# Performance work log

Hardware: AMD Instinct MI355X
Metric: run time of the kernel (lower is better)

## Reference

```python
import jax, jax.numpy as jnp
import numpy as np

B, T, J, C, H = 128, 512, 21, 3, 64


def setup_inputs() -> dict:
    key = jax.random.key(0)
    ks = jax.random.split(key, 14)
    x = jax.random.normal(ks[0], (B, T, J, C), dtype=jnp.float32)
    # Fixed skeleton-like adjacency buffer: symmetric, self-loops, row-normalized.
    A = (jax.random.uniform(ks[1], (J, J)) < 0.15).astype(jnp.float32)
    A = jnp.clip(A + A.T, 0.0, 1.0) + jnp.eye(J, dtype=jnp.float32)
    A = A / A.sum(axis=1, keepdims=True)
    s = 0.05
    W1 = jax.random.normal(ks[2], (H, C), jnp.float32) * s
    b1 = jnp.zeros((H,), jnp.float32)
    W2 = jax.random.normal(ks[3], (H, H), jnp.float32) * s
    b2 = jnp.zeros((H,), jnp.float32)
    Wa = jax.random.normal(ks[4], (1, H), jnp.float32) * s
    ba = jnp.zeros((1,), jnp.float32)
    W_ih = jax.random.normal(ks[5], (3 * H, J * H), jnp.float32) * s
    b_ih = jnp.zeros((3 * H,), jnp.float32)
    W_hh = jax.random.normal(ks[6], (3 * H, H), jnp.float32) * s
    b_hh = jnp.zeros((3 * H,), jnp.float32)
    W_head = jax.random.normal(ks[7], (J * C, H), jnp.float32) * s
    b_head = jnp.zeros((J * C,), jnp.float32)
    return {"x": x, "A": A, "W1": W1, "b1": b1, "W2": W2, "b2": b2,
            "Wa": Wa, "ba": ba, "W_ih": W_ih, "b_ih": b_ih,
            "W_hh": W_hh, "b_hh": b_hh, "W_head": W_head, "b_head": b_head}


def _gcn(A, x, W, b):
    # aggregated = einsum('ij,btjc->btic'); then Linear + ReLU
    agg = jnp.einsum('ij,btjc->btic', A, x)
    return jax.nn.relu(agg @ W.T + b)


def reference(x, A, W1, b1, W2, b2, Wa, ba, W_ih, b_ih, W_hh, b_hh, W_head, b_head):
    h = _gcn(A, x, W1, b1)            # (B,T,J,H)
    h = _gcn(A, h, W2, b2)            # (B,T,J,H)
    # Spatial attention: per-node score, mean over time, softmax over joints
    scores = (h @ Wa.T + ba).mean(axis=1)        # (B,J,1)
    attn = jax.nn.softmax(scores, axis=1)        # (B,J,1)
    h = h * attn[:, None]                        # (B,T,J,H)
    b_, t_, j_, c_ = h.shape
    seq = h.reshape(b_, t_, j_ * c_)             # (B,T,J*H)
    # GRU (PyTorch convention). Precompute input projections outside the scan.
    xproj = seq @ W_ih.T + b_ih                  # (B,T,3H)
    h0 = jnp.zeros((b_, H), xproj.dtype)

    def step(hprev, xp):
        gh = hprev @ W_hh.T + b_hh
        xr, xz, xn = jnp.split(xp, 3, axis=-1)
        hr, hz, hn = jnp.split(gh, 3, axis=-1)
        r = jax.nn.sigmoid(xr + hr)
        z = jax.nn.sigmoid(xz + hz)
        n = jnp.tanh(xn + r * hn)
        hnew = (1.0 - z) * n + z * hprev
        return hnew, None

    hT, _ = jax.lax.scan(step, h0, jnp.swapaxes(xproj, 0, 1))  # last hidden state
    out = hT @ W_head.T + b_head                 # (B, J*C)
    return out, attn.squeeze(-1)
```

## Files before the change

kernel.cpp:

```cpp
#include <hip/hip_runtime.h>
#include <cstdint>
#include <cstddef>

#define NB 128
#define NT 512
#define NJ 21
#define NC 3
#define NH 64
#define JH 1344
#define G3 192
#define OUT0 (NB*NJ*NC)
#define FB 4

typedef __attribute__((ext_vector_type(8))) __bf16 bf16x8;
typedef __attribute__((ext_vector_type(4))) float f32x4;

__device__ __forceinline__ float bf2f(unsigned short u) {
  union { unsigned int i; float f; } v; v.i = ((unsigned int)u) << 16; return v.f;
}
__device__ __forceinline__ unsigned short f2bf(float f) {
  union { float f; unsigned int i; } v; v.f = f;
  unsigned int x = v.i;
  unsigned int lsb = (x >> 16) & 1u;
  x += 0x7fffu + lsb;
  return (unsigned short)(x >> 16);
}
__device__ __forceinline__ unsigned int pk_bf16(float lo, float hi) {
  unsigned int r;
  asm("v_cvt_pk_bf16_f32 %0, %1, %2" : "=v"(r) : "v"(lo), "v"(hi));
  return r;
}
__device__ __forceinline__ unsigned int scale2(unsigned int u, float s) {
  float lo = __uint_as_float(u << 16);
  float hi = __uint_as_float(u & 0xffff0000u);
  return pk_bf16(lo * s, hi * s);
}

__global__ __launch_bounds__(256) void k0_convw(
    const float* __restrict__ W, unsigned short* __restrict__ Wbf) {
  const int ti = blockIdx.x*256 + threadIdx.x;
  const float4 v = ((const float4*)W)[ti];
  uint2 o;
  o.x = (unsigned int)f2bf(v.x) | ((unsigned int)f2bf(v.y) << 16);
  o.y = (unsigned int)f2bf(v.z) | ((unsigned int)f2bf(v.w) << 16);
  ((uint2*)Wbf)[ti] = o;
}

__global__ __launch_bounds__(256, 2) void k1_fused(
    const float* __restrict__ x, const float* __restrict__ A,
    const float* __restrict__ W1, const float* __restrict__ b1,
    const float* __restrict__ W2, const float* __restrict__ b2,
    const float* __restrict__ Wa,
    unsigned short* __restrict__ h2out, float* __restrict__ scorepart) {
  __shared__ unsigned short h1s[FB*32*72];
  __shared__ unsigned short us[FB*64*40];
  __shared__ unsigned short w2s[64*72];
  __shared__ unsigned short adjs[32*40];
  __shared__ unsigned short h2st[FB*NJ*72];
  __shared__ float afs[NJ*NJ];
  __shared__ float xs[4][64];
  __shared__ float ags[4][64];
  __shared__ float spred[4][NJ];

  const int tid = threadIdx.x;
  const int w = tid >> 6, l = tid & 63;
  const int q = l >> 4, r = l & 15;
  const int b = blockIdx.x >> 7, ch = blockIdx.x & 127;
  const int t0 = ch * FB;

  for (int i = tid; i < NJ*NJ; i += 256) afs[i] = A[i];
  for (int i = tid; i < 1024; i += 256) {
    const int ii = i >> 5, jj = i & 31;
    adjs[ii*40 + jj] = (ii < NJ && jj < NJ) ? f2bf(A[ii*NJ + jj]) : (unsigned short)0;
  }
  {
    const int h = tid & 63, qd = tid >> 6;
    const int g0 = qd * 16;
#pragma unroll
    for (int e = 0; e < 16; e += 2) {
      const float v0 = W2[h*64 + g0 + e], v1 = W2[h*64 + g0 + e + 1];
      ((unsigned int*)w2s)[h*36 + ((g0 + e) >> 1)] = pk_bf16(v0, v1);
    }
  }
#pragma unroll
  for (int j = NJ; j < 32; ++j)
    ((unsigned int*)h1s)[(w*32 + j)*36 + (l & 31)] = 0u;

  const float w1r0 = W1[l*3+0], w1r1 = W1[l*3+1], w1r2 = W1[l*3+2];
  const float b1h = b1[l];
  float b2v[4][4], wav[4][4];
#pragma unroll
  for (int mt = 0; mt < 4; ++mt)
#pragma unroll
    for (int rg = 0; rg < 4; ++rg) {
      const int h = mt*16 + q*4 + rg;
      b2v[mt][rg] = b2[h]; wav[mt][rg] = Wa[h];
    }
  __syncthreads();

  {
    const size_t fr = (size_t)(b*NT + t0 + w);
    if (l < NJ*NC) xs[w][l] = x[fr*(NJ*NC) + l];
    if (l < NJ*NC) {
      const int ji = l / 3, c = l - ji*3;
      float s = 0.f;
#pragma unroll
      for (int j = 0; j < NJ; ++j) s += afs[ji*NJ + j] * xs[w][j*3 + c];
      ags[w][l] = s;
    }
#pragma unroll
    for (int j = 0; j < NJ; ++j) {
      float v = b1h + w1r0*ags[w][j*3+0] + w1r1*ags[w][j*3+1] + w1r2*ags[w][j*3+2];
      v = fmaxf(v, 0.f);
      h1s[(w*32 + j)*72 + l] = f2bf(v);
    }
  }
  __syncthreads();

  bf16x8 bw[2][4];
#pragma unroll
  for (int ks = 0; ks < 2; ++ks)
#pragma unroll
    for (int nt = 0; nt < 4; ++nt)
      bw[ks][nt] = *(const bf16x8*)(&w2s[(nt*16 + r)*72 + (ks*4 + q)*8]);
  f32x4 acc1[2][4];
#pragma unroll
  for (int i = 0; i < 2; ++i)
#pragma unroll
    for (int j2 = 0; j2 < 4; ++j2) acc1[i][j2] = (f32x4)0.f;
#pragma unroll
  for (int mti = 0; mti < 2; ++mti) {
    const int row = (w*2 + mti)*16 + r;
#pragma unroll
    for (int ks = 0; ks < 2; ++ks) {
      const bf16x8 af = *(const bf16x8*)(&h1s[row*72 + (ks*4 + q)*8]);
#pragma unroll
      for (int nt = 0; nt < 4; ++nt)
        acc1[mti][nt] = __builtin_amdgcn_mfma_f32_16x16x32_bf16(af, bw[ks][nt], acc1[mti][nt], 0,0,0);
    }
  }
#pragma unroll
  for (int mti = 0; mti < 2; ++mti)
#pragma unroll
    for (int nt = 0; nt < 4; ++nt) {
      const int h = nt*16 + r;
#pragma unroll
      for (int rp = 0; rp < 2; ++rp) {
        const int jp = mti*16 + q*4 + rp*2;
        ((unsigned int*)us)[(w*64 + h)*20 + (jp >> 1)] =
            pk_bf16(acc1[mti][nt][rp*2], acc1[mti][nt][rp*2+1]);
      }
    }
  __syncthreads();

  bf16x8 badj[2];
#pragma unroll
  for (int nt = 0; nt < 2; ++nt)
    badj[nt] = *(const bf16x8*)(&adjs[(nt*16 + r)*40 + q*8]);
  f32x4 acc2[4][2];
#pragma unroll
  for (int i = 0; i < 4; ++i) { acc2[i][0] = (f32x4)0.f; acc2[i][1] = (f32x4)0.f; }
#pragma unroll
  for (int mt = 0; mt < 4; ++mt) {
    const int h = mt*16 + r;
    const bf16x8 af = *(const bf16x8*)(&us[(w*64 + h)*40 + q*8]);
#pragma unroll
    for (int nt = 0; nt < 2; ++nt)
      acc2[mt][nt] = __builtin_amdgcn_mfma_f32_16x16x32_bf16(af, badj[nt], acc2[mt][nt], 0,0,0);
  }
  float sp0 = 0.f, sp1 = 0.f;
#pragma unroll
  for (int nt = 0; nt < 2; ++nt) {
    const int i = nt*16 + r;
    if (i < NJ) {
#pragma unroll
      for (int mt = 0; mt < 4; ++mt)
#pragma unroll
        for (int rp = 0; rp < 2; ++rp) {
          const int h0 = mt*16 + q*4 + rp*2;
          const float v0 = fmaxf(acc2[mt][nt][rp*2]   + b2v[mt][rp*2],   0.f);
          const float v1 = fmaxf(acc2[mt][nt][rp*2+1] + b2v[mt][rp*2+1], 0.f);
          if (nt == 0) sp0 += v0*wav[mt][rp*2] + v1*wav[mt][rp*2+1];
          else         sp1 += v0*wav[mt][rp*2] + v1*wav[mt][rp*2+1];
          ((unsigned int*)h2st)[(w*NJ + i)*36 + (h0 >> 1)] = pk_bf16(v0, v1);
        }
    }
  }
  sp0 += __shfl_xor(sp0, 16); sp0 += __shfl_xor(sp0, 32);
  sp1 += __shfl_xor(sp1, 16); sp1 += __shfl_xor(sp1, 32);
  if (l < 16) spred[w][l] = sp0;
  if (l < 5)  spred[w][16 + l] = sp1;
  __syncthreads();

  if (tid < NJ)
    scorepart[((size_t)b*128 + ch)*NJ + tid] =
      spred[0][tid] + spred[1][tid] + spred[2][tid] + spred[3][tid];

  const size_t gbase = (size_t)(b*NT + t0) * JH;
  for (int cid = tid; cid < FB*NJ*8; cid += 256) {
    const int f = cid / (NJ*8), rem = cid - f*(NJ*8);
    const int i = rem >> 3, p = rem & 7;
    const uint4 v = *(const uint4*)(&h2st[(f*NJ + i)*72 + p*8]);
    *(uint4*)(&h2out[gbase + (size_t)f*JH + i*64 + p*8]) = v;
  }
}

__global__ __launch_bounds__(64) void k2_attn(
    const float* __restrict__ scorepart, float* __restrict__ attn,
    float* __restrict__ out_attn) {
  __shared__ float ss[NJ];
  const int b = blockIdx.x, tid = threadIdx.x;
  if (tid < NJ) {
    float s = 0.f;
    for (int ch = 0; ch < 128; ++ch) s += scorepart[(b*128 + ch)*NJ + tid];
    ss[tid] = s * (1.0f/NT);
  }
  __syncthreads();
  float m = -1e30f;
  for (int j = 0; j < NJ; ++j) m = fmaxf(m, ss[j]);
  float sum = 0.f;
  for (int j = 0; j < NJ; ++j) sum += expf(ss[j] - m);
  if (tid < NJ) {
    float a = expf(ss[tid] - m) / sum;
    attn[b*NJ + tid] = a;
    out_attn[b*NJ + tid] = a;
  }
}

__global__ __launch_bounds__(256, 2) void k3_xproj_mfma(
    const unsigned short* __restrict__ h2, const unsigned short* __restrict__ Wbf,
    const float* __restrict__ b_ih, const float* __restrict__ b_hh,
    const float* __restrict__ attn, float* __restrict__ xproj) {
  __shared__ unsigned short Abuf[2][128*32];
  __shared__ unsigned short Bbuf[2][192*32];
  const int tid = threadIdx.x;
  const int w = tid >> 6, l = tid & 63;
  const int lq = l >> 4, lr = l & 15;
  const int blk = blockIdx.x;
  const int b = blk >> 2;
  const int t0 = (blk & 3) << 7;
  const int wm = w >> 1, wn = w & 1;

  const unsigned short* gA[2]; int ldsA[2];
#pragma unroll
  for (int i = 0; i < 2; ++i) {
    const int lc = tid*2 + i, rr = lc >> 2, j = lc & 3;
    gA[i] = h2 + (size_t)(b*NT + t0 + rr)*JH + j*8;
    ldsA[i] = rr*32 + ((j ^ ((rr>>1)&3)) << 3);
  }
  const unsigned short* gB[3]; int ldsB[3];
#pragma unroll
  for (int i = 0; i < 3; ++i) {
    const int lc = tid + 256*i, g = lc >> 2, j = lc & 3;
    gB[i] = Wbf + (size_t)g*JH + j*8;
    ldsB[i] = g*32 + ((j ^ ((g>>1)&3)) << 3);
  }
  int aoff[4], boff[6];
#pragma unroll
  for (int mt = 0; mt < 4; ++mt) {
    const int row = wm*64 + mt*16 + lr;
    aoff[mt] = row*32 + ((lq ^ ((row>>1)&3)) << 3);
  }
#pragma unroll
  for (int nt = 0; nt < 6; ++nt) {
    const int g = wn*96 + nt*16 + lr;
    boff[nt] = g*32 + ((lq ^ ((g>>1)&3)) << 3);
  }

  f32x4 acc[4][6];
#pragma unroll
  for (int mt = 0; mt < 4; ++mt)
#pragma unroll
    for (int nt = 0; nt < 6; ++nt) acc[mt][nt] = (f32x4)0.f;

  {
    const float s = attn[b*NJ + 0];
#pragma unroll
    for (int i = 0; i < 2; ++i)
      *(uint4*)(&Abuf[0][ldsA[i]]) = *(const uint4*)(gA[i]);
#pragma unroll
    for (int i = 0; i < 3; ++i) {
      uint4 v = *(const uint4*)(gB[i]);
      v.x = scale2(v.x, s); v.y = scale2(v.y, s);
      v.z = scale2(v.z, s); v.w = scale2(v.w, s);
      *(uint4*)(&Bbuf[0][ldsB[i]]) = v;
    }
  }
  __syncthreads();

  for (int ks = 0; ks < 42; ++ks) {
    const int cur = ks & 1;
    uint4 av0, av1, bv0, bv1, bv2;
    if (ks < 41) {
      const int kk = (ks+1)*32;
      av0 = *(const uint4*)(gA[0] + kk);
      av1 = *(const uint4*)(gA[1] + kk);
      bv0 = *(const uint4*)(gB[0] + kk);
      bv1 = *(const uint4*)(gB[1] + kk);
      bv2 = *(const uint4*)(gB[2] + kk);
    }
    bf16x8 af[4], bfr[6];
#pragma unroll
    for (int mt = 0; mt < 4; ++mt) af[mt] = *(const bf16x8*)(&Abuf[cur][aoff[mt]]);
#pragma unroll
    for (int nt = 0; nt < 6; ++nt) bfr[nt] = *(const bf16x8*)(&Bbuf[cur][boff[nt]]);
#pragma unroll
    for (int mt = 0; mt < 4; ++mt)
#pragma unroll
      for (int nt = 0; nt < 6; ++nt)
        acc[mt][nt] = __builtin_amdgcn_mfma_f32_16x16x32_bf16(af[mt], bfr[nt], acc[mt][nt], 0, 0, 0);
    if (ks < 41) {
      const float s = attn[b*NJ + ((ks+1) >> 1)];
      *(uint4*)(&Abuf[cur^1][ldsA[0]]) = av0;
      *(uint4*)(&Abuf[cur^1][ldsA[1]]) = av1;
      uint4 v;
      v = bv0; v.x = scale2(v.x, s); v.y = scale2(v.y, s); v.z = scale2(v.z, s); v.w = scale2(v.w, s);
      *(uint4*)(&Bbuf[cur^1][ldsB[0]]) = v;
      v = bv1; v.x = scale2(v.x, s); v.y = scale2(v.y, s); v.z = scale2(v.z, s); v.w = scale2(v.w, s);
      *(uint4*)(&Bbuf[cur^1][ldsB[1]]) = v;
      v = bv2; v.x = scale2(v.x, s); v.y = scale2(v.y, s); v.z = scale2(v.z, s); v.w = scale2(v.w, s);
      *(uint4*)(&Bbuf[cur^1][ldsB[2]]) = v;
    }
    __syncthreads();
  }

  float bias[6];
#pragma unroll
  for (int nt = 0; nt < 6; ++nt) {
    const int g = wn*96 + nt*16 + lr;
    bias[nt] = b_ih[g] + (g < 2*NH ? b_hh[g] : 0.f);
  }
#pragma unroll
  for (int mt = 0; mt < 4; ++mt)
#pragma unroll
    for (int nt = 0; nt < 6; ++nt) {
      const int g = wn*96 + nt*16 + lr;
      const int trow = t0 + wm*64 + mt*16 + lq*4;
      float4 o;
      o.x = acc[mt][nt][0] + bias[nt];
      o.y = acc[mt][nt][1] + bias[nt];
      o.z = acc[mt][nt][2] + bias[nt];
      o.w = acc[mt][nt][3] + bias[nt];
      *(float4*)(&xproj[(size_t)(b*G3 + g)*NT + trow]) = o;
    }
}

__global__ __launch_bounds__(512, 1) void k4_gru_mfma(
    const float* __restrict__ xproj, const float* __restrict__ W_hh,
    const float* __restrict__ b_hh, float* __restrict__ hT) {
  __shared__ __align__(16) uint4 hb4[2][2][4][16];
  const int tid = threadIdx.x;
  const int w = tid >> 6, l = tid & 63, q = l >> 4, r15 = l & 15;
  const int b0 = blockIdx.x * 16;

  for (int i = tid; i < 256; i += 512) ((uint4*)hb4)[i] = uint4{0u,0u,0u,0u};

  bf16x8 afr[2][2];
  int chv[2]; float bn_[2];
#pragma unroll
  for (int i = 0; i < 2; ++i) {
    const int mt = 2*w + i;
    const int gate = r15 & 3;
    const int cha = 8*(mt >> 1) + 2*(r15 >> 2) + (mt & 1);
#pragma unroll
    for (int ks = 0; ks < 2; ++ks) {
      union { bf16x8 v; unsigned int u[4]; } tu;
      if (gate < 3) {
        const float* src = W_hh + (size_t)(gate*NH + cha)*NH + ks*32 + q*8;
        const float4 a = *(const float4*)(src);
        const float4 b = *(const float4*)(src + 4);
        tu.u[0] = pk_bf16(a.x, a.y); tu.u[1] = pk_bf16(a.z, a.w);
        tu.u[2] = pk_bf16(b.x, b.y); tu.u[3] = pk_bf16(b.z, b.w);
      } else {
        tu.u[0]=0u; tu.u[1]=0u; tu.u[2]=0u; tu.u[3]=0u;
      }
      afr[i][ks] = tu.v;
    }
    chv[i] = 8*w + 2*q + i;
    bn_[i] = b_hh[2*NH + chv[i]];
  }
  const int half = w >> 2, qblk = w & 3;

  const float* xrow[2][3];
#pragma unroll
  for (int i = 0; i < 2; ++i)
#pragma unroll
    for (int e = 0; e < 3; ++e)
      xrow[i][e] = xproj + (size_t)((b0 + r15)*G3 + e*NH + chv[i]) * NT;

  float hprev[2] = {0.f, 0.f};
  __syncthreads();

  f32x4 cur[2][3], nxt[2][3];
#pragma unroll
  for (int i = 0; i < 2; ++i)
#pragma unroll
    for (int e = 0; e < 3; ++e) { cur[i][e] = *(const f32x4*)(xrow[i][e]); nxt[i][e] = cur[i][e]; }

  for (int tg = 0; tg < NT; tg += 4) {
    if (tg + 4 < NT) {
#pragma unroll
      for (int i = 0; i < 2; ++i)
#pragma unroll
        for (int e = 0; e < 3; ++e) nxt[i][e] = *(const f32x4*)(xrow[i][e] + tg + 4);
    }
#pragma unroll
    for (int p = 0; p < 4; ++p) {
      const int rb = p & 1, wb = rb ^ 1;
      const bf16x8 bh0 = *(const bf16x8*)(&hb4[rb][0][q][r15]);
      const bf16x8 bh1 = *(const bf16x8*)(&hb4[rb][1][q][r15]);
      f32x4 acc[2];
      acc[0] = (f32x4)0.f; acc[1] = (f32x4)0.f;
      acc[0] = __builtin_amdgcn_mfma_f32_16x16x32_bf16(afr[0][0], bh0, acc[0], 0,0,0);
      acc[1] = __builtin_amdgcn_mfma_f32_16x16x32_bf16(afr[1][0], bh0, acc[1], 0,0,0);
      acc[0] = __builtin_amdgcn_mfma_f32_16x16x32_bf16(afr[0][1], bh1, acc[0], 0,0,0);
      acc[1] = __builtin_amdgcn_mfma_f32_16x16x32_bf16(afr[1][1], bh1, acc[1], 0,0,0);
      float hnew[2];
#pragma unroll
      for (int i = 0; i < 2; ++i) {
        const float xr = cur[i][0][p], xz = cur[i][1][p], xn = cur[i][2][p];
        const float hn = acc[i][2] + bn_[i];
        const float rr = __builtin_amdgcn_rcpf(1.f + __expf(-(xr + acc[i][0])));
        const float zz = __builtin_amdgcn_rcpf(1.f + __expf(-(xz + acc[i][1])));
        const float nx = xn + rr*hn;
        const float nn = 2.f*__builtin_amdgcn_rcpf(1.f + __expf(-2.f*nx)) - 1.f;
        hnew[i] = nn + zz*(hprev[i] - nn);
        hprev[i] = hnew[i];
      }
      ((unsigned int*)&hb4[wb][half][qblk][r15])[q] = pk_bf16(hnew[0], hnew[1]);
      asm volatile("s_waitcnt lgkmcnt(0)" ::: "memory");
      __builtin_amdgcn_s_barrier();
    }
#pragma unroll
    for (int i = 0; i < 2; ++i)
#pragma unroll
      for (int e = 0; e < 3; ++e) cur[i][e] = nxt[i][e];
  }

#pragma unroll
  for (int i = 0; i < 2; ++i)
    hT[(size_t)(b0 + r15)*NH + chv[i]] = hprev[i];
}

__global__ __launch_bounds__(256) void k5_head(
    const float* __restrict__ hT, const float* __restrict__ W_head,
    const float* __restrict__ b_head, float* __restrict__ out) {
  const int idx = blockIdx.x*256 + threadIdx.x;
  if (idx >= NB*63) return;
  const int b = idx / 63, rr = idx % 63;
  const float* hv = hT + b*NH;
  const float* wr = W_head + rr*NH;
  float acc = b_head[rr];
#pragma unroll
  for (int k = 0; k < NH; ++k) acc += hv[k]*wr[k];
  out[idx] = acc;
}

extern "C" void kernel_launch(void* const* d_in, const int* in_sizes, int n_in,
                              void* d_out, int out_size, void* d_ws, size_t ws_size,
                              hipStream_t stream) {
  const float* x      = (const float*)d_in[0];
  const float* A      = (const float*)d_in[1];
  const float* W1     = (const float*)d_in[2];
  const float* b1     = (const float*)d_in[3];
  const float* W2     = (const float*)d_in[4];
  const float* b2     = (const float*)d_in[5];
  const float* Wa     = (const float*)d_in[6];
  const float* W_ih   = (const float*)d_in[8];
  const float* b_ih   = (const float*)d_in[9];
  const float* W_hh   = (const float*)d_in[10];
  const float* b_hh   = (const float*)d_in[11];
  const float* W_head = (const float*)d_in[12];
  const float* b_head = (const float*)d_in[13];
  float* out = (float*)d_out;

  char* ws = (char*)d_ws;
  size_t off = 0;
  unsigned short* h2 = (unsigned short*)(ws + off); off += (size_t)NB*NT*JH*2;
  float* scorepart   = (float*)(ws + off);          off += (size_t)NB*128*NJ*4;
  float* attn        = (float*)(ws + off);          off += (size_t)NB*NJ*4;
  off = (off + 15) & ~(size_t)15;
  float* xproj       = (float*)(ws + off);          off += (size_t)NB*NT*G3*4;
  float* hT          = (float*)(ws + off);          off += (size_t)NB*NH*4;
  off = (off + 15) & ~(size_t)15;
  unsigned short* Wbf = (unsigned short*)(ws + off); off += (size_t)G3*JH*2;

  k0_convw<<<dim3(252),       256, 0, stream>>>(W_ih, Wbf);
  k1_fused<<<dim3(NB*128),    256, 0, stream>>>(x, A, W1, b1, W2, b2, Wa, h2, scorepart);
  k2_attn<<<dim3(NB),          64, 0, stream>>>(scorepart, attn, out + OUT0);
  k3_xproj_mfma<<<dim3(512),  256, 0, stream>>>(h2, Wbf, b_ih, b_hh, attn, xproj);
  k4_gru_mfma<<<dim3(8),      512, 0, stream>>>(xproj, W_hh, b_hh, hT);
  k5_head<<<dim3((NB*63 + 255)/256), 256, 0, stream>>>(hT, W_head, b_head, out);
}
```

Baseline: 500.4 us.

## Fuse xproj GEMM and GRU scan into one kernel with chunked counter handoff

```diff
diff --git a/kernel.cpp b/kernel.cpp
--- a/kernel.cpp
+++ b/kernel.cpp
@@ -227,219 +227,243 @@
   }
 }
 
-__global__ __launch_bounds__(256, 2) void k3_xproj_mfma(
+struct SK3 {
+  unsigned short Ab[2][2][32*32];
+  unsigned short Bb[2][192*32];
+};
+struct SK4 { uint4 hb4[2][2][4][16]; };
+union SMem34 { SK3 k3; SK4 k4; };
+
+__global__ __launch_bounds__(512, 4) void k34_fused(
     const unsigned short* __restrict__ h2, const unsigned short* __restrict__ Wbf,
     const float* __restrict__ b_ih, const float* __restrict__ b_hh,
-    const float* __restrict__ attn, float* __restrict__ xproj) {
-  __shared__ unsigned short Abuf[2][128*32];
-  __shared__ unsigned short Bbuf[2][192*32];
+    const float* __restrict__ attn, float* __restrict__ xproj,
+    const float* __restrict__ W_hh, float* __restrict__ hT,
+    int* __restrict__ cnt) {
+  __shared__ SMem34 sm;
   const int tid = threadIdx.x;
-  const int w = tid >> 6, l = tid & 63;
+
+  if (blockIdx.x < 8) {
+    const int g = blockIdx.x;
+    const int w = tid >> 6, l = tid & 63, q = l >> 4, r15 = l & 15;
+    const int b0 = g * 16;
+
+    for (int i = tid; i < 256; i += 512)
+      ((uint4*)sm.k4.hb4)[i] = uint4{0u,0u,0u,0u};
+
+    bf16x8 afr[2][2];
+    int chv[2]; float bn_[2];
+#pragma unroll
+    for (int i = 0; i < 2; ++i) {
+      const int mt = 2*w + i;
+      const int gate = r15 & 3;
+      const int cha = 8*(mt >> 1) + 2*(r15 >> 2) + (mt & 1);
+#pragma unroll
+      for (int ks = 0; ks < 2; ++ks) {
+        union { bf16x8 v; unsigned int u[4]; } tu;
+        if (gate < 3) {
+          const float* src = W_hh + (size_t)(gate*NH + cha)*NH + ks*32 + q*8;
+          const float4 a = *(const float4*)(src);
+          const float4 b = *(const float4*)(src + 4);
+          tu.u[0] = pk_bf16(a.x, a.y); tu.u[1] = pk_bf16(a.z, a.w);
+          tu.u[2] = pk_bf16(b.x, b.y); tu.u[3] = pk_bf16(b.z, b.w);
+        } else {
+          tu.u[0]=0u; tu.u[1]=0u; tu.u[2]=0u; tu.u[3]=0u;
+        }
+        afr[i][ks] = tu.v;
+      }
+      chv[i] = 8*w + 2*q + i;
+      bn_[i] = b_hh[2*NH + chv[i]];
+    }
+    const int half = w >> 2, qblk = w & 3;
+
+    const float* xrow[2][3];
+#pragma unroll
+    for (int i = 0; i < 2; ++i)
+#pragma unroll
+      for (int e = 0; e < 3; ++e)
+        xrow[i][e] = xproj + (size_t)((b0 + r15)*G3 + e*NH + chv[i]) * NT;
+
+    if (tid == 0) {
+      while (__hip_atomic_load(&cnt[g*4 + 0], __ATOMIC_ACQUIRE,
+                               __HIP_MEMORY_SCOPE_AGENT) < 32)
+        __builtin_amdgcn_s_sleep(2);
+    }
+    __syncthreads();
+
+    float hprev[2] = {0.f, 0.f};
+    f32x4 cur[2][3], nxt[2][3];
+#pragma unroll
+    for (int i = 0; i < 2; ++i)
+#pragma unroll
+      for (int e = 0; e < 3; ++e) { cur[i][e] = *(const f32x4*)(xrow[i][e]); nxt[i][e] = cur[i][e]; }
+
+    for (int tg = 0; tg < NT; tg += 4) {
+      if (tg + 4 < NT && ((tg + 4) & 127) == 0) {
+        const int c = (tg + 4) >> 7;
+        if (tid == 0) {
+          while (__hip_atomic_load(&cnt[g*4 + c], __ATOMIC_ACQUIRE,
+                                   __HIP_MEMORY_SCOPE_AGENT) < 32)
+            __builtin_amdgcn_s_sleep(2);
+        }
+        __syncthreads();
+      }
+      if (tg + 4 < NT) {
+#pragma unroll
+        for (int i = 0; i < 2; ++i)
+#pragma unroll
+          for (int e = 0; e < 3; ++e) nxt[i][e] = *(const f32x4*)(xrow[i][e] + tg + 4);
+      }
+#pragma unroll
+      for (int p = 0; p < 4; ++p) {
+        const int rb = p & 1, wb = rb ^ 1;
+        const bf16x8 bh0 = *(const bf16x8*)(&sm.k4.hb4[rb][0][q][r15]);
+        const bf16x8 bh1 = *(const bf16x8*)(&sm.k4.hb4[rb][1][q][r15]);
+        f32x4 acc[2];
+        acc[0] = (f32x4)0.f; acc[1] = (f32x4)0.f;
+        acc[0] = __builtin_amdgcn_mfma_f32_16x16x32_bf16(afr[0][0], bh0, acc[0], 0,0,0);
+        acc[1] = __builtin_amdgcn_mfma_f32_16x16x32_bf16(afr[1][0], bh0, acc[1], 0,0,0);
+        acc[0] = __builtin_amdgcn_mfma_f32_16x16x32_bf16(afr[0][1], bh1, acc[0], 0,0,0);
+        acc[1] = __builtin_amdgcn_mfma_f32_16x16x32_bf16(afr[1][1], bh1, acc[1], 0,0,0);
+        float hnew[2];
+#pragma unroll
+        for (int i = 0; i < 2; ++i) {
+          const float xr = cur[i][0][p], xz = cur[i][1][p], xn = cur[i][2][p];
+          const float hn = acc[i][2] + bn_[i];
+          const float rr = __builtin_amdgcn_rcpf(1.f + __expf(-(xr + acc[i][0])));
+          const float zz = __builtin_amdgcn_rcpf(1.f + __expf(-(xz + acc[i][1])));
+          const float nx = xn + rr*hn;
+          const float nn = 2.f*__builtin_amdgcn_rcpf(1.f + __expf(-2.f*nx)) - 1.f;
+          hnew[i] = nn + zz*(hprev[i] - nn);
+          hprev[i] = hnew[i];
+        }
+        ((unsigned int*)&sm.k4.hb4[wb][half][qblk][r15])[q] = pk_bf16(hnew[0], hnew[1]);
+        asm volatile("s_waitcnt lgkmcnt(0)" ::: "memory");
+        __builtin_amdgcn_s_barrier();
+        __builtin_amdgcn_sched_barrier(0);
+      }
+#pragma unroll
+      for (int i = 0; i < 2; ++i)
+#pragma unroll
+        for (int e = 0; e < 3; ++e) cur[i][e] = nxt[i][e];
+    }
+
+#pragma unroll
+    for (int i = 0; i < 2; ++i)
+      hT[(size_t)(b0 + r15)*NH + chv[i]] = hprev[i];
+    return;
+  }
+
+  const int kb = blockIdx.x - 8;
+  const int b = kb >> 1, hf = kb & 1;
+  const int sub = tid >> 8, stid = tid & 255;
+  const int w = (tid >> 6) & 3, l = tid & 63;
   const int lq = l >> 4, lr = l & 15;
-  const int blk = blockIdx.x;
-  const int b = blk >> 2;
-  const int t0 = (blk & 3) << 7;
   const int wm = w >> 1, wn = w & 1;
 
-  const unsigned short* gA[2]; int ldsA[2];
-#pragma unroll
-  for (int i = 0; i < 2; ++i) {
-    const int lc = tid*2 + i, rr = lc >> 2, j = lc & 3;
-    gA[i] = h2 + (size_t)(b*NT + t0 + rr)*JH + j*8;
-    ldsA[i] = rr*32 + ((j ^ ((rr>>1)&3)) << 3);
-  }
-  const unsigned short* gB[3]; int ldsB[3];
-#pragma unroll
-  for (int i = 0; i < 3; ++i) {
-    const int lc = tid + 256*i, g = lc >> 2, j = lc & 3;
-    gB[i] = Wbf + (size_t)g*JH + j*8;
-    ldsB[i] = g*32 + ((j ^ ((g>>1)&3)) << 3);
-  }
-  int aoff[4], boff[6];
-#pragma unroll
-  for (int mt = 0; mt < 4; ++mt) {
-    const int row = wm*64 + mt*16 + lr;
-    aoff[mt] = row*32 + ((lq ^ ((row>>1)&3)) << 3);
-  }
+  const unsigned short* gA0 = nullptr; int ldsA = 0;
+  if (stid < 128) {
+    const int rr = stid >> 2, j = stid & 3;
+    gA0 = h2 + (size_t)(b*NT + rr)*JH + j*8;
+    ldsA = rr*32 + ((j ^ ((rr >> 1) & 3)) << 3);
+  }
+  const unsigned short* gB0; int ldsB0;
+  { const int g = tid >> 2, j = tid & 3;
+    gB0 = Wbf + (size_t)g*JH + j*8;
+    ldsB0 = g*32 + ((j ^ ((g >> 1) & 3)) << 3); }
+  const unsigned short* gB1 = nullptr; int ldsB1 = 0;
+  if (tid < 256) {
+    const int lc = 512 + tid, g = lc >> 2, j = lc & 3;
+    gB1 = Wbf + (size_t)g*JH + j*8;
+    ldsB1 = g*32 + ((j ^ ((g >> 1) & 3)) << 3);
+  }
+  int aoff, boff[6];
+  { const int row = wm*16 + lr;
+    aoff = row*32 + ((lq ^ ((row >> 1) & 3)) << 3); }
 #pragma unroll
   for (int nt = 0; nt < 6; ++nt) {
     const int g = wn*96 + nt*16 + lr;
-    boff[nt] = g*32 + ((lq ^ ((g>>1)&3)) << 3);
-  }
-
-  f32x4 acc[4][6];
-#pragma unroll
-  for (int mt = 0; mt < 4; ++mt)
-#pragma unroll
-    for (int nt = 0; nt < 6; ++nt) acc[mt][nt] = (f32x4)0.f;
-
-  {
-    const float s = attn[b*NJ + 0];
-#pragma unroll
-    for (int i = 0; i < 2; ++i)
-      *(uint4*)(&Abuf[0][ldsA[i]]) = *(const uint4*)(gA[i]);
-#pragma unroll
-    for (int i = 0; i < 3; ++i) {
-      uint4 v = *(const uint4*)(gB[i]);
-      v.x = scale2(v.x, s); v.y = scale2(v.y, s);
-      v.z = scale2(v.z, s); v.w = scale2(v.w, s);
-      *(uint4*)(&Bbuf[0][ldsB[i]]) = v;
-    }
-  }
-  __syncthreads();
-
-  for (int ks = 0; ks < 42; ++ks) {
-    const int cur = ks & 1;
-    uint4 av0, av1, bv0, bv1, bv2;
-    if (ks < 41) {
-      const int kk = (ks+1)*32;
-      av0 = *(const uint4*)(gA[0] + kk);
-      av1 = *(const uint4*)(gA[1] + kk);
-      bv0 = *(const uint4*)(gB[0] + kk);
-      bv1 = *(const uint4*)(gB[1] + kk);
-      bv2 = *(const uint4*)(gB[2] + kk);
-    }
-    bf16x8 af[4], bfr[6];
-#pragma unroll
-    for (int mt = 0; mt < 4; ++mt) af[mt] = *(const bf16x8*)(&Abuf[cur][aoff[mt]]);
-#pragma unroll
-    for (int nt = 0; nt < 6; ++nt) bfr[nt] = *(const bf16x8*)(&Bbuf[cur][boff[nt]]);
-#pragma unroll
-    for (int mt = 0; mt < 4; ++mt)
-#pragma unroll
-      for (int nt = 0; nt < 6; ++nt)
-        acc[mt][nt] = __builtin_amdgcn_mfma_f32_16x16x32_bf16(af[mt], bfr[nt], acc[mt][nt], 0, 0, 0);
-    if (ks < 41) {
-      const float s = attn[b*NJ + ((ks+1) >> 1)];
-      *(uint4*)(&Abuf[cur^1][ldsA[0]]) = av0;
-      *(uint4*)(&Abuf[cur^1][ldsA[1]]) = av1;
-      uint4 v;
-      v = bv0; v.x = scale2(v.x, s); v.y = scale2(v.y, s); v.z = scale2(v.z, s); v.w = scale2(v.w, s);
-      *(uint4*)(&Bbuf[cur^1][ldsB[0]]) = v;
-      v = bv1; v.x = scale2(v.x, s); v.y = scale2(v.y, s); v.z = scale2(v.z, s); v.w = scale2(v.w, s);
-      *(uint4*)(&Bbuf[cur^1][ldsB[1]]) = v;
-      v = bv2; v.x = scale2(v.x, s); v.y = scale2(v.y, s); v.z = scale2(v.z, s); v.w = scale2(v.w, s);
-      *(uint4*)(&Bbuf[cur^1][ldsB[2]]) = v;
-    }
-    __syncthreads();
-  }
-
+    boff[nt] = g*32 + ((lq ^ ((g >> 1) & 3)) << 3);
+  }
   float bias[6];
 #pragma unroll
   for (int nt = 0; nt < 6; ++nt) {
     const int g = wn*96 + nt*16 + lr;
     bias[nt] = b_ih[g] + (g < 2*NH ? b_hh[g] : 0.f);
   }
-#pragma unroll
-  for (int mt = 0; mt < 4; ++mt)
+
+  for (int c = 0; c < 4; ++c) {
+    const int R0 = c*128 + hf*64 + sub*32;
+    const unsigned short* gAp = gA0 + (size_t)R0*JH;
+
+    f32x4 acc[6];
+#pragma unroll
+    for (int nt = 0; nt < 6; ++nt) acc[nt] = (f32x4)0.f;
+
+    {
+      const float s = attn[b*NJ + 0];
+      if (stid < 128) *(uint4*)(&sm.k3.Ab[sub][0][ldsA]) = *(const uint4*)(gAp);
+      uint4 v = *(const uint4*)(gB0);
+      v.x = scale2(v.x, s); v.y = scale2(v.y, s);
+      v.z = scale2(v.z, s); v.w = scale2(v.w, s);
+      *(uint4*)(&sm.k3.Bb[0][ldsB0]) = v;
+      if (tid < 256) {
+        uint4 u = *(const uint4*)(gB1);
+        u.x = scale2(u.x, s); u.y = scale2(u.y, s);
+        u.z = scale2(u.z, s); u.w = scale2(u.w, s);
+        *(uint4*)(&sm.k3.Bb[0][ldsB1]) = u;
+      }
+    }
+    __syncthreads();
+
+    for (int ks = 0; ks < 42; ++ks) {
+      const int curb = ks & 1;
+      uint4 av, bv0, bv1;
+      if (ks < 41) {
+        const int kk = (ks+1)*32;
+        if (stid < 128) av = *(const uint4*)(gAp + kk);
+        bv0 = *(const uint4*)(gB0 + kk);
+        if (tid < 256) bv1 = *(const uint4*)(gB1 + kk);
+      }
+      const bf16x8 af = *(const bf16x8*)(&sm.k3.Ab[sub][curb][aoff]);
+      bf16x8 bfr[6];
+#pragma unroll
+      for (int nt = 0; nt < 6; ++nt) bfr[nt] = *(const bf16x8*)(&sm.k3.Bb[curb][boff[nt]]);
+#pragma unroll
+      for (int nt = 0; nt < 6; ++nt)
+        acc[nt] = __builtin_amdgcn_mfma_f32_16x16x32_bf16(af, bfr[nt], acc[nt], 0, 0, 0);
+      if (ks < 41) {
+        const float s = attn[b*NJ + ((ks+1) >> 1)];
+        if (stid < 128) *(uint4*)(&sm.k3.Ab[sub][curb^1][ldsA]) = av;
+        bv0.x = scale2(bv0.x, s); bv0.y = scale2(bv0.y, s);
+        bv0.z = scale2(bv0.z, s); bv0.w = scale2(bv0.w, s);
+        *(uint4*)(&sm.k3.Bb[curb^1][ldsB0]) = bv0;
+        if (tid < 256) {
+          bv1.x = scale2(bv1.x, s); bv1.y = scale2(bv1.y, s);
+          bv1.z = scale2(bv1.z, s); bv1.w = scale2(bv1.w, s);
+          *(uint4*)(&sm.k3.Bb[curb^1][ldsB1]) = bv1;
+        }
+      }
+      __syncthreads();
+    }
+
 #pragma unroll
     for (int nt = 0; nt < 6; ++nt) {
       const int g = wn*96 + nt*16 + lr;
-      const int trow = t0 + wm*64 + mt*16 + lq*4;
+      const int trow = R0 + wm*16 + lq*4;
       float4 o;
-      o.x = acc[mt][nt][0] + bias[nt];
-      o.y = acc[mt][nt][1] + bias[nt];
-      o.z = acc[mt][nt][2] + bias[nt];
-      o.w = acc[mt][nt][3] + bias[nt];
+      o.x = acc[nt][0] + bias[nt];
+      o.y = acc[nt][1] + bias[nt];
+      o.z = acc[nt][2] + bias[nt];
+      o.w = acc[nt][3] + bias[nt];
       *(float4*)(&xproj[(size_t)(b*G3 + g)*NT + trow]) = o;
     }
-}
-
-__global__ __launch_bounds__(512, 1) void k4_gru_mfma(
-    const float* __restrict__ xproj, const float* __restrict__ W_hh,
-    const float* __restrict__ b_hh, float* __restrict__ hT) {
-  __shared__ __align__(16) uint4 hb4[2][2][4][16];
-  const int tid = threadIdx.x;
-  const int w = tid >> 6, l = tid & 63, q = l >> 4, r15 = l & 15;
-  const int b0 = blockIdx.x * 16;
-
-  for (int i = tid; i < 256; i += 512) ((uint4*)hb4)[i] = uint4{0u,0u,0u,0u};
-
-  bf16x8 afr[2][2];
-  int chv[2]; float bn_[2];
-#pragma unroll
-  for (int i = 0; i < 2; ++i) {
-    const int mt = 2*w + i;
-    const int gate = r15 & 3;
-    const int cha = 8*(mt >> 1) + 2*(r15 >> 2) + (mt & 1);
-#pragma unroll
-    for (int ks = 0; ks < 2; ++ks) {
-      union { bf16x8 v; unsigned int u[4]; } tu;
-      if (gate < 3) {
-        const float* src = W_hh + (size_t)(gate*NH + cha)*NH + ks*32 + q*8;
-        const float4 a = *(const float4*)(src);
-        const float4 b = *(const float4*)(src + 4);
-        tu.u[0] = pk_bf16(a.x, a.y); tu.u[1] = pk_bf16(a.z, a.w);
-        tu.u[2] = pk_bf16(b.x, b.y); tu.u[3] = pk_bf16(b.z, b.w);
-      } else {
-        tu.u[0]=0u; tu.u[1]=0u; tu.u[2]=0u; tu.u[3]=0u;
-      }
-      afr[i][ks] = tu.v;
-    }
-    chv[i] = 8*w + 2*q + i;
-    bn_[i] = b_hh[2*NH + chv[i]];
-  }
-  const int half = w >> 2, qblk = w & 3;
-
-  const float* xrow[2][3];
-#pragma unroll
-  for (int i = 0; i < 2; ++i)
-#pragma unroll
-    for (int e = 0; e < 3; ++e)
-      xrow[i][e] = xproj + (size_t)((b0 + r15)*G3 + e*NH + chv[i]) * NT;
-
-  float hprev[2] = {0.f, 0.f};
-  __syncthreads();
-
-  f32x4 cur[2][3], nxt[2][3];
-#pragma unroll
-  for (int i = 0; i < 2; ++i)
-#pragma unroll
-    for (int e = 0; e < 3; ++e) { cur[i][e] = *(const f32x4*)(xrow[i][e]); nxt[i][e] = cur[i][e]; }
-
-  for (int tg = 0; tg < NT; tg += 4) {
-    if (tg + 4 < NT) {
-#pragma unroll
-      for (int i = 0; i < 2; ++i)
-#pragma unroll
-        for (int e = 0; e < 3; ++e) nxt[i][e] = *(const f32x4*)(xrow[i][e] + tg + 4);
-    }
-#pragma unroll
-    for (int p = 0; p < 4; ++p) {
-      const int rb = p & 1, wb = rb ^ 1;
-      const bf16x8 bh0 = *(const bf16x8*)(&hb4[rb][0][q][r15]);
-      const bf16x8 bh1 = *(const bf16x8*)(&hb4[rb][1][q][r15]);
-      f32x4 acc[2];
-      acc[0] = (f32x4)0.f; acc[1] = (f32x4)0.f;
-      acc[0] = __builtin_amdgcn_mfma_f32_16x16x32_bf16(afr[0][0], bh0, acc[0], 0,0,0);
-      acc[1] = __builtin_amdgcn_mfma_f32_16x16x32_bf16(afr[1][0], bh0, acc[1], 0,0,0);
-      acc[0] = __builtin_amdgcn_mfma_f32_16x16x32_bf16(afr[0][1], bh1, acc[0], 0,0,0);
-      acc[1] = __builtin_amdgcn_mfma_f32_16x16x32_bf16(afr[1][1], bh1, acc[1], 0,0,0);
-      float hnew[2];
-#pragma unroll
-      for (int i = 0; i < 2; ++i) {
-        const float xr = cur[i][0][p], xz = cur[i][1][p], xn = cur[i][2][p];
-        const float hn = acc[i][2] + bn_[i];
-        const float rr = __builtin_amdgcn_rcpf(1.f + __expf(-(xr + acc[i][0])));
-        const float zz = __builtin_amdgcn_rcpf(1.f + __expf(-(xz + acc[i][1])));
-        const float nx = xn + rr*hn;
-        const float nn = 2.f*__builtin_amdgcn_rcpf(1.f + __expf(-2.f*nx)) - 1.f;
-        hnew[i] = nn + zz*(hprev[i] - nn);
-        hprev[i] = hnew[i];
-      }
-      ((unsigned int*)&hb4[wb][half][qblk][r15])[q] = pk_bf16(hnew[0], hnew[1]);
-      asm volatile("s_waitcnt lgkmcnt(0)" ::: "memory");
-      __builtin_amdgcn_s_barrier();
-    }
-#pragma unroll
-    for (int i = 0; i < 2; ++i)
-#pragma unroll
-      for (int e = 0; e < 3; ++e) cur[i][e] = nxt[i][e];
-  }
-
-#pragma unroll
-  for (int i = 0; i < 2; ++i)
-    hT[(size_t)(b0 + r15)*NH + chv[i]] = hprev[i];
+    __threadfence();
+    __syncthreads();
+    if (tid == 0)
+      __hip_atomic_fetch_add(&cnt[(b >> 4)*4 + c], 1, __ATOMIC_RELEASE,
+                             __HIP_MEMORY_SCOPE_AGENT);
+  }
 }
 
 __global__ __launch_bounds__(256) void k5_head(
@@ -484,11 +508,13 @@
   float* hT          = (float*)(ws + off);          off += (size_t)NB*NH*4;
   off = (off + 15) & ~(size_t)15;
   unsigned short* Wbf = (unsigned short*)(ws + off); off += (size_t)G3*JH*2;
-
+  off = (off + 15) & ~(size_t)15;
+  int* cnt           = (int*)(ws + off);            off += 32*sizeof(int);
+
+  hipMemsetAsync(cnt, 0, 32*sizeof(int), stream);
   k0_convw<<<dim3(252),       256, 0, stream>>>(W_ih, Wbf);
   k1_fused<<<dim3(NB*128),    256, 0, stream>>>(x, A, W1, b1, W2, b2, Wa, h2, scorepart);
   k2_attn<<<dim3(NB),          64, 0, stream>>>(scorepart, attn, out + OUT0);
-  k3_xproj_mfma<<<dim3(512),  256, 0, stream>>>(h2, Wbf, b_ih, b_hh, attn, xproj);
-  k4_gru_mfma<<<dim3(8),      512, 0, stream>>>(xproj, W_hh, b_hh, hT);
+  k34_fused<<<dim3(264),      512, 0, stream>>>(h2, Wbf, b_ih, b_hh, attn, xproj, W_hh, hT, cnt);
   k5_head<<<dim3((NB*63 + 255)/256), 256, 0, stream>>>(hT, W_head, b_head, out);
 }
```

Result: slower. 720.8 us (+44.1%).

## Process two batch groups per GRU block to amortize per-step barriers

Applied to the files above, without the earlier changes.

```diff
diff --git a/kernel.cpp b/kernel.cpp
--- a/kernel.cpp
+++ b/kernel.cpp
@@ -348,12 +348,16 @@
 __global__ __launch_bounds__(512, 1) void k4_gru_mfma(
     const float* __restrict__ xproj, const float* __restrict__ W_hh,
     const float* __restrict__ b_hh, float* __restrict__ hT) {
-  __shared__ __align__(16) uint4 hb4[2][2][4][16];
+  __shared__ __align__(16) uint4 hbA[2][2][4][16];
+  __shared__ __align__(16) uint4 hbB[2][2][4][16];
   const int tid = threadIdx.x;
   const int w = tid >> 6, l = tid & 63, q = l >> 4, r15 = l & 15;
-  const int b0 = blockIdx.x * 16;
-
-  for (int i = tid; i < 256; i += 512) ((uint4*)hb4)[i] = uint4{0u,0u,0u,0u};
+  const int b0 = blockIdx.x * 32;
+
+  for (int i = tid; i < 256; i += 512) {
+    ((uint4*)hbA)[i] = uint4{0u,0u,0u,0u};
+    ((uint4*)hbB)[i] = uint4{0u,0u,0u,0u};
+  }
 
   bf16x8 afr[2][2];
   int chv[2]; float bn_[2];
@@ -381,65 +385,98 @@
   }
   const int half = w >> 2, qblk = w & 3;
 
-  const float* xrow[2][3];
+  const float* xrowA[2][3]; const float* xrowB[2][3];
 #pragma unroll
   for (int i = 0; i < 2; ++i)
 #pragma unroll
-    for (int e = 0; e < 3; ++e)
-      xrow[i][e] = xproj + (size_t)((b0 + r15)*G3 + e*NH + chv[i]) * NT;
-
-  float hprev[2] = {0.f, 0.f};
-  __syncthreads();
-
-  f32x4 cur[2][3], nxt[2][3];
+    for (int e = 0; e < 3; ++e) {
+      xrowA[i][e] = xproj + (size_t)((b0 + r15)*G3 + e*NH + chv[i]) * NT;
+      xrowB[i][e] = xproj + (size_t)((b0 + 16 + r15)*G3 + e*NH + chv[i]) * NT;
+    }
+
+  float hpA[2] = {0.f, 0.f}, hpB[2] = {0.f, 0.f};
+  __syncthreads();
+
+  f32x4 curA[2][3], nxtA[2][3], curB[2][3], nxtB[2][3];
 #pragma unroll
   for (int i = 0; i < 2; ++i)
 #pragma unroll
-    for (int e = 0; e < 3; ++e) { cur[i][e] = *(const f32x4*)(xrow[i][e]); nxt[i][e] = cur[i][e]; }
+    for (int e = 0; e < 3; ++e) {
+      curA[i][e] = *(const f32x4*)(xrowA[i][e]); nxtA[i][e] = curA[i][e];
+      curB[i][e] = *(const f32x4*)(xrowB[i][e]); nxtB[i][e] = curB[i][e];
+    }
 
   for (int tg = 0; tg < NT; tg += 4) {
     if (tg + 4 < NT) {
 #pragma unroll
       for (int i = 0; i < 2; ++i)
 #pragma unroll
-        for (int e = 0; e < 3; ++e) nxt[i][e] = *(const f32x4*)(xrow[i][e] + tg + 4);
+        for (int e = 0; e < 3; ++e) {
+          nxtA[i][e] = *(const f32x4*)(xrowA[i][e] + tg + 4);
+          nxtB[i][e] = *(const f32x4*)(xrowB[i][e] + tg + 4);
+        }
     }
 #pragma unroll
     for (int p = 0; p < 4; ++p) {
       const int rb = p & 1, wb = rb ^ 1;
-      const bf16x8 bh0 = *(const bf16x8*)(&hb4[rb][0][q][r15]);
-      const bf16x8 bh1 = *(const bf16x8*)(&hb4[rb][1][q][r15]);
-      f32x4 acc[2];
-      acc[0] = (f32x4)0.f; acc[1] = (f32x4)0.f;
-      acc[0] = __builtin_amdgcn_mfma_f32_16x16x32_bf16(afr[0][0], bh0, acc[0], 0,0,0);
-      acc[1] = __builtin_amdgcn_mfma_f32_16x16x32_bf16(afr[1][0], bh0, acc[1], 0,0,0);
-      acc[0] = __builtin_amdgcn_mfma_f32_16x16x32_bf16(afr[0][1], bh1, acc[0], 0,0,0);
-      acc[1] = __builtin_amdgcn_mfma_f32_16x16x32_bf16(afr[1][1], bh1, acc[1], 0,0,0);
-      float hnew[2];
+      const bf16x8 a0 = *(const bf16x8*)(&hbA[rb][0][q][r15]);
+      const bf16x8 a1 = *(const bf16x8*)(&hbA[rb][1][q][r15]);
+      const bf16x8 b0v = *(const bf16x8*)(&hbB[rb][0][q][r15]);
+      const bf16x8 b1v = *(const bf16x8*)(&hbB[rb][1][q][r15]);
+      f32x4 accA[2], accB[2];
+      accA[0] = (f32x4)0.f; accA[1] = (f32x4)0.f;
+      accB[0] = (f32x4)0.f; accB[1] = (f32x4)0.f;
+      accA[0] = __builtin_amdgcn_mfma_f32_16x16x32_bf16(afr[0][0], a0, accA[0], 0,0,0);
+      accA[1] = __builtin_amdgcn_mfma_f32_16x16x32_bf16(afr[1][0], a0, accA[1], 0,0,0);
+      accB[0] = __builtin_amdgcn_mfma_f32_16x16x32_bf16(afr[0][0], b0v, accB[0], 0,0,0);
+      accB[1] = __builtin_amdgcn_mfma_f32_16x16x32_bf16(afr[1][0], b0v, accB[1], 0,0,0);
+      accA[0] = __builtin_amdgcn_mfma_f32_16x16x32_bf16(afr[0][1], a1, accA[0], 0,0,0);
+      accA[1] = __builtin_amdgcn_mfma_f32_16x16x32_bf16(afr[1][1], a1, accA[1], 0,0,0);
+      accB[0] = __builtin_amdgcn_mfma_f32_16x16x32_bf16(afr[0][1], b1v, accB[0], 0,0,0);
+      accB[1] = __builtin_amdgcn_mfma_f32_16x16x32_bf16(afr[1][1], b1v, accB[1], 0,0,0);
+      float hnA[2], hnB[2];
 #pragma unroll
       for (int i = 0; i < 2; ++i) {
-        const float xr = cur[i][0][p], xz = cur[i][1][p], xn = cur[i][2][p];
-        const float hn = acc[i][2] + bn_[i];
-        const float rr = __builtin_amdgcn_rcpf(1.f + __expf(-(xr + acc[i][0])));
-        const float zz = __builtin_amdgcn_rcpf(1.f + __expf(-(xz + acc[i][1])));
-        const float nx = xn + rr*hn;
-        const float nn = 2.f*__builtin_amdgcn_rcpf(1.f + __expf(-2.f*nx)) - 1.f;
-        hnew[i] = nn + zz*(hprev[i] - nn);
-        hprev[i] = hnew[i];
+        {
+          const float xr = curA[i][0][p], xz = curA[i][1][p], xn = curA[i][2][p];
+          const float hn = accA[i][2] + bn_[i];
+          const float rr = __builtin_amdgcn_rcpf(1.f + __expf(-(xr + accA[i][0])));
+          const float zz = __builtin_amdgcn_rcpf(1.f + __expf(-(xz + accA[i][1])));
+          const float nx = xn + rr*hn;
+          const float nn = 2.f*__builtin_amdgcn_rcpf(1.f + __expf(-2.f*nx)) - 1.f;
+          hnA[i] = nn + zz*(hpA[i] - nn);
+          hpA[i] = hnA[i];
+        }
+        {
+          const float xr = curB[i][0][p], xz = curB[i][1][p], xn = curB[i][2][p];
+          const float hn = accB[i][2] + bn_[i];
+          const float rr = __builtin_amdgcn_rcpf(1.f + __expf(-(xr + accB[i][0])));
+          const float zz = __builtin_amdgcn_rcpf(1.f + __expf(-(xz + accB[i][1])));
+          const float nx = xn + rr*hn;
+          const float nn = 2.f*__builtin_amdgcn_rcpf(1.f + __expf(-2.f*nx)) - 1.f;
+          hnB[i] = nn + zz*(hpB[i] - nn);
+          hpB[i] = hnB[i];
+        }
       }
-      ((unsigned int*)&hb4[wb][half][qblk][r15])[q] = pk_bf16(hnew[0], hnew[1]);
+      ((unsigned int*)&hbA[wb][half][qblk][r15])[q] = pk_bf16(hnA[0], hnA[1]);
+      ((unsigned int*)&hbB[wb][half][qblk][r15])[q] = pk_bf16(hnB[0], hnB[1]);
       asm volatile("s_waitcnt lgkmcnt(0)" ::: "memory");
       __builtin_amdgcn_s_barrier();
     }
 #pragma unroll
     for (int i = 0; i < 2; ++i)
 #pragma unroll
-      for (int e = 0; e < 3; ++e) cur[i][e] = nxt[i][e];
-  }
-
-#pragma unroll
-  for (int i = 0; i < 2; ++i)
-    hT[(size_t)(b0 + r15)*NH + chv[i]] = hprev[i];
+      for (int e = 0; e < 3; ++e) {
+        curA[i][e] = nxtA[i][e];
+        curB[i][e] = nxtB[i][e];
+      }
+  }
+
+#pragma unroll
+  for (int i = 0; i < 2; ++i) {
+    hT[(size_t)(b0 + r15)*NH + chv[i]]      = hpA[i];
+    hT[(size_t)(b0 + 16 + r15)*NH + chv[i]] = hpB[i];
+  }
 }
 
 __global__ __launch_bounds__(256) void k5_head(
@@ -489,6 +526,6 @@
   k1_fused<<<dim3(NB*128),    256, 0, stream>>>(x, A, W1, b1, W2, b2, Wa, h2, scorepart);
   k2_attn<<<dim3(NB),          64, 0, stream>>>(scorepart, attn, out + OUT0);
   k3_xproj_mfma<<<dim3(512),  256, 0, stream>>>(h2, Wbf, b_ih, b_hh, attn, xproj);
-  k4_gru_mfma<<<dim3(8),      512, 0, stream>>>(xproj, W_hh, b_hh, hT);
+  k4_gru_mfma<<<dim3(4),      512, 0, stream>>>(xproj, W_hh, b_hh, hT);
   k5_head<<<dim3((NB*63 + 255)/256), 256, 0, stream>>>(hT, W_head, b_head, out);
 }
```

New measurement: 798.8 us. 59.6% more time.

## Split GRU recurrence across 16 waves with one channel per lane

Applied to the files above, without the earlier changes.

```diff
diff --git a/kernel.cpp b/kernel.cpp
--- a/kernel.cpp
+++ b/kernel.cpp
@@ -345,7 +345,7 @@
     }
 }
 
-__global__ __launch_bounds__(512, 1) void k4_gru_mfma(
+__global__ __launch_bounds__(1024, 1) void k4_gru_mfma(
     const float* __restrict__ xproj, const float* __restrict__ W_hh,
     const float* __restrict__ b_hh, float* __restrict__ hT) {
   __shared__ __align__(16) uint4 hb4[2][2][4][16];
@@ -353,93 +353,71 @@
   const int w = tid >> 6, l = tid & 63, q = l >> 4, r15 = l & 15;
   const int b0 = blockIdx.x * 16;
 
-  for (int i = tid; i < 256; i += 512) ((uint4*)hb4)[i] = uint4{0u,0u,0u,0u};
-
-  bf16x8 afr[2][2];
-  int chv[2]; float bn_[2];
-#pragma unroll
-  for (int i = 0; i < 2; ++i) {
-    const int mt = 2*w + i;
-    const int gate = r15 & 3;
-    const int cha = 8*(mt >> 1) + 2*(r15 >> 2) + (mt & 1);
-#pragma unroll
-    for (int ks = 0; ks < 2; ++ks) {
-      union { bf16x8 v; unsigned int u[4]; } tu;
-      if (gate < 3) {
-        const float* src = W_hh + (size_t)(gate*NH + cha)*NH + ks*32 + q*8;
-        const float4 a = *(const float4*)(src);
-        const float4 b = *(const float4*)(src + 4);
-        tu.u[0] = pk_bf16(a.x, a.y); tu.u[1] = pk_bf16(a.z, a.w);
-        tu.u[2] = pk_bf16(b.x, b.y); tu.u[3] = pk_bf16(b.z, b.w);
-      } else {
-        tu.u[0]=0u; tu.u[1]=0u; tu.u[2]=0u; tu.u[3]=0u;
-      }
-      afr[i][ks] = tu.v;
-    }
-    chv[i] = 8*w + 2*q + i;
-    bn_[i] = b_hh[2*NH + chv[i]];
-  }
-  const int half = w >> 2, qblk = w & 3;
-
-  const float* xrow[2][3];
-#pragma unroll
-  for (int i = 0; i < 2; ++i)
-#pragma unroll
-    for (int e = 0; e < 3; ++e)
-      xrow[i][e] = xproj + (size_t)((b0 + r15)*G3 + e*NH + chv[i]) * NT;
-
-  float hprev[2] = {0.f, 0.f};
-  __syncthreads();
-
-  f32x4 cur[2][3], nxt[2][3];
-#pragma unroll
-  for (int i = 0; i < 2; ++i)
-#pragma unroll
-    for (int e = 0; e < 3; ++e) { cur[i][e] = *(const f32x4*)(xrow[i][e]); nxt[i][e] = cur[i][e]; }
+  for (int i = tid; i < 256; i += 1024) ((uint4*)hb4)[i] = uint4{0u,0u,0u,0u};
+
+  bf16x8 afr[2];
+  const int gate = r15 & 3;
+  const int cha = 8*(w >> 1) + 2*(r15 >> 2) + (w & 1);
+#pragma unroll
+  for (int ks = 0; ks < 2; ++ks) {
+    union { bf16x8 v; unsigned int u[4]; } tu;
+    if (gate < 3) {
+      const float* src = W_hh + (size_t)(gate*NH + cha)*NH + ks*32 + q*8;
+      const float4 a = *(const float4*)(src);
+      const float4 b = *(const float4*)(src + 4);
+      tu.u[0] = pk_bf16(a.x, a.y); tu.u[1] = pk_bf16(a.z, a.w);
+      tu.u[2] = pk_bf16(b.x, b.y); tu.u[3] = pk_bf16(b.z, b.w);
+    } else {
+      tu.u[0]=0u; tu.u[1]=0u; tu.u[2]=0u; tu.u[3]=0u;
+    }
+    afr[ks] = tu.v;
+  }
+  const int chv = 8*(w >> 1) + 2*q + (w & 1);
+  const float bn_ = b_hh[2*NH + chv];
+  const int wh = w >> 3, wq = (w >> 1) & 3, wb16 = q*2 + (w & 1);
+
+  const float* xrow[3];
+#pragma unroll
+  for (int e = 0; e < 3; ++e)
+    xrow[e] = xproj + (size_t)((b0 + r15)*G3 + e*NH + chv) * NT;
+
+  float hprev = 0.f;
+  __syncthreads();
+
+  f32x4 cur[3], nxt[3];
+#pragma unroll
+  for (int e = 0; e < 3; ++e) { cur[e] = *(const f32x4*)(xrow[e]); nxt[e] = cur[e]; }
 
   for (int tg = 0; tg < NT; tg += 4) {
     if (tg + 4 < NT) {
 #pragma unroll
-      for (int i = 0; i < 2; ++i)
-#pragma unroll
-        for (int e = 0; e < 3; ++e) nxt[i][e] = *(const f32x4*)(xrow[i][e] + tg + 4);
+      for (int e = 0; e < 3; ++e) nxt[e] = *(const f32x4*)(xrow[e] + tg + 4);
     }
 #pragma unroll
     for (int p = 0; p < 4; ++p) {
-      const int rb = p & 1, wb = rb ^ 1;
+      const int rb = p & 1, wbuf = rb ^ 1;
       const bf16x8 bh0 = *(const bf16x8*)(&hb4[rb][0][q][r15]);
       const bf16x8 bh1 = *(const bf16x8*)(&hb4[rb][1][q][r15]);
-      f32x4 acc[2];
-      acc[0] = (f32x4)0.f; acc[1] = (f32x4)0.f;
-      acc[0] = __builtin_amdgcn_mfma_f32_16x16x32_bf16(afr[0][0], bh0, acc[0], 0,0,0);
-      acc[1] = __builtin_amdgcn_mfma_f32_16x16x32_bf16(afr[1][0], bh0, acc[1], 0,0,0);
-      acc[0] = __builtin_amdgcn_mfma_f32_16x16x32_bf16(afr[0][1], bh1, acc[0], 0,0,0);
-      acc[1] = __builtin_amdgcn_mfma_f32_16x16x32_bf16(afr[1][1], bh1, acc[1], 0,0,0);
-      float hnew[2];
-#pragma unroll
-      for (int i = 0; i < 2; ++i) {
-        const float xr = cur[i][0][p], xz = cur[i][1][p], xn = cur[i][2][p];
-        const float hn = acc[i][2] + bn_[i];
-        const float rr = __builtin_amdgcn_rcpf(1.f + __expf(-(xr + acc[i][0])));
-        const float zz = __builtin_amdgcn_rcpf(1.f + __expf(-(xz + acc[i][1])));
-        const float nx = xn + rr*hn;
-        const float nn = 2.f*__builtin_amdgcn_rcpf(1.f + __expf(-2.f*nx)) - 1.f;
-        hnew[i] = nn + zz*(hprev[i] - nn);
-        hprev[i] = hnew[i];
-      }
-      ((unsigned int*)&hb4[wb][half][qblk][r15])[q] = pk_bf16(hnew[0], hnew[1]);
+      f32x4 acc = (f32x4)0.f;
+      acc = __builtin_amdgcn_mfma_f32_16x16x32_bf16(afr[0], bh0, acc, 0,0,0);
+      acc = __builtin_amdgcn_mfma_f32_16x16x32_bf16(afr[1], bh1, acc, 0,0,0);
+      const float xr = cur[0][p], xz = cur[1][p], xn = cur[2][p];
+      const float hn = acc[2] + bn_;
+      const float rr = __builtin_amdgcn_rcpf(1.f + __expf(-(xr + acc[0])));
+      const float zz = __builtin_amdgcn_rcpf(1.f + __expf(-(xz + acc[1])));
+      const float nx = xn + rr*hn;
+      const float nn = 2.f*__builtin_amdgcn_rcpf(1.f + __expf(-2.f*nx)) - 1.f;
+      const float hnew = nn + zz*(hprev - nn);
+      hprev = hnew;
+      ((unsigned short*)&hb4[wbuf][wh][wq][r15])[wb16] = f2bf(hnew);
       asm volatile("s_waitcnt lgkmcnt(0)" ::: "memory");
       __builtin_amdgcn_s_barrier();
     }
 #pragma unroll
-    for (int i = 0; i < 2; ++i)
-#pragma unroll
-      for (int e = 0; e < 3; ++e) cur[i][e] = nxt[i][e];
-  }
-
-#pragma unroll
-  for (int i = 0; i < 2; ++i)
-    hT[(size_t)(b0 + r15)*NH + chv[i]] = hprev[i];
+    for (int e = 0; e < 3; ++e) cur[e] = nxt[e];
+  }
+
+  hT[(size_t)(b0 + r15)*NH + chv] = hprev;
 }
 
 __global__ __launch_bounds__(256) void k5_head(
@@ -489,6 +467,6 @@
   k1_fused<<<dim3(NB*128),    256, 0, stream>>>(x, A, W1, b1, W2, b2, Wa, h2, scorepart);
   k2_attn<<<dim3(NB),          64, 0, stream>>>(scorepart, attn, out + OUT0);
   k3_xproj_mfma<<<dim3(512),  256, 0, stream>>>(h2, Wbf, b_ih, b_hh, attn, xproj);
-  k4_gru_mfma<<<dim3(8),      512, 0, stream>>>(xproj, W_hh, b_hh, hT);
+  k4_gru_mfma<<<dim3(8),     1024, 0, stream>>>(xproj, W_hh, b_hh, hT);
   k5_head<<<dim3((NB*63 + 255)/256), 256, 0, stream>>>(hT, W_head, b_head, out);
 }
```

Result: no change. 495.1 us, median of 2 (-1.1%).
